# Performance work log

Hardware: AMD Instinct MI355X
Metric: run time of the kernel (lower is better)

## Reference

```python
import jax, jax.numpy as jnp
import numpy as np

T, L, B, M, E, H, A, HID, OBS = 8, 2, 512, 128, 512, 8, 16, 1024, 64
DH = E // H


def _ln(x, s, b):
    m = jnp.mean(x, axis=-1, keepdims=True)
    v = jnp.var(x, axis=-1, keepdims=True)
    return (x - m) * jax.lax.rsqrt(v + 1e-6) * s + b


def _mlp(z, w1, b1, w2, b2, w3, b3):
    z = jax.nn.relu(z @ w1 + b1)
    z = jax.nn.relu(z @ w2 + b2)
    return z @ w3 + b3


def setup_inputs() -> dict:
    key = jax.random.key(0)
    ks = jax.random.split(key, 20)
    r = lambda i, shape: jax.random.normal(ks[i], shape, jnp.float32) * 0.02
    return dict(
        memories=jax.random.normal(ks[0], (B, L, M, E), jnp.float32),
        obs=jax.random.normal(ks[1], (B, OBS), jnp.float32),
        We=r(2, (T, OBS, E)), be=jnp.zeros((T, E), jnp.float32),
        Wq=r(3, (T, L, E, E)), Wk=r(4, (T, L, E, E)), Wv=r(5, (T, L, E, E)),
        Wo=r(6, (T, L, E, E)), bo=jnp.zeros((T, L, E), jnp.float32),
        W1=r(7, (T, L, E, E)), b1=jnp.zeros((T, L, E), jnp.float32),
        W2=r(8, (T, L, E, E)), b2=jnp.zeros((T, L, E), jnp.float32),
        ln1_s=jnp.ones((T, L, E), jnp.float32), ln1_b=jnp.zeros((T, L, E), jnp.float32),
        ln2_s=jnp.ones((T, L, E), jnp.float32), ln2_b=jnp.zeros((T, L, E), jnp.float32),
        aW1=r(9, (T, E, HID)), ab1=jnp.zeros((T, HID), jnp.float32),
        aW2=r(10, (T, HID, HID)), ab2=jnp.zeros((T, HID), jnp.float32),
        aW3=r(11, (T, HID, A)), ab3=jnp.zeros((T, A), jnp.float32),
        cW1=r(12, (T, E, HID)), cb1=jnp.zeros((T, HID), jnp.float32),
        cW2=r(13, (T, HID, HID)), cb2=jnp.zeros((T, HID), jnp.float32),
        cW3=r(14, (T, HID, 1)), cb3=jnp.zeros((T, 1), jnp.float32),
        state_skills=jax.random.randint(ks[15], (B,), 0, T),
        mask=jnp.ones((B, M), dtype=bool),
    )


def reference(memories, obs, We, be, Wq, Wk, Wv, Wo, bo, W1, b1, W2, b2,
              ln1_s, ln1_b, ln2_s, ln2_b, aW1, ab1, aW2, ab2, aW3, ab3,
              cW1, cb1, cW2, cb2, cW3, cb3, state_skills, mask):
    scale = 1.0 / np.sqrt(DH)
    # current-step token is always attendable -> append True column
    fmask = jnp.concatenate([mask, jnp.ones((B, 1), dtype=bool)], axis=1)  # [B, M+1]
    xs, mems = [], []
    for t in range(T):  # dense compute over ALL tasks (as in the original)
        h = obs @ We[t] + be[t]  # [B, E]
        layer_mems = []
        for l in range(L):
            layer_mems.append(h)  # TrXL-style: memory_out = layer inputs
            kv = jnp.concatenate([memories[:, l], h[:, None, :]], axis=1)  # [B, M+1, E]
            qn = _ln(h, ln1_s[t, l], ln1_b[t, l])
            kn = _ln(kv, ln1_s[t, l], ln1_b[t, l])
            q = (qn @ Wq[t, l]).reshape(B, H, DH)
            k = (kn @ Wk[t, l]).reshape(B, M + 1, H, DH)
            v = (kn @ Wv[t, l]).reshape(B, M + 1, H, DH)
            s = jnp.einsum('bhd,bshd->bhs', q, k) * scale
            s = jnp.where(fmask[:, None, :], s, -1e9)
            p = jax.nn.softmax(s, axis=-1)
            o = jnp.einsum('bhs,bshd->bhd', p, v).reshape(B, E) @ Wo[t, l] + bo[t, l]
            h = h + o
            hn = _ln(h, ln2_s[t, l], ln2_b[t, l])
            h = h + jax.nn.relu(hn @ W1[t, l] + b1[t, l]) @ W2[t, l] + b2[t, l]
        xs.append(h)
        mems.append(jnp.stack(layer_mems, axis=1))  # [B, L, E]
    x_all = jnp.stack(xs, axis=1)       # [B, T, E]
    mem_all = jnp.stack(mems, axis=1)   # [B, T, L, E]
    onehot = jnp.eye(T, dtype=x_all.dtype)[state_skills]  # [B, T]
    x = jnp.sum(x_all * onehot[:, :, None], axis=1)                 # [B, E]
    memory_out = jnp.sum(mem_all * onehot[:, :, None, None], axis=1)  # [B, L, E]
    actor = jnp.stack([_mlp(x, aW1[t], ab1[t], aW2[t], ab2[t], aW3[t], ab3[t]) for t in range(T)], axis=1)   # [B, T, A]
    critic = jnp.stack([_mlp(x, cW1[t], cb1[t], cW2[t], cb2[t], cW3[t], cb3[t]) for t in range(T)], axis=1)  # [B, T, 1]
    logits = jnp.sum(actor * onehot[:, :, None], axis=1)                    # [B, A]
    values = jnp.sum(critic * onehot[:, :, None], axis=1).squeeze(-1)       # [B]
    return logits, values, memory_out
```

## Files before the change

kernel.cpp:

```cpp
#include <hip/hip_runtime.h>

#define TT    8
#define LLAY  2
#define BB    512
#define MM    128
#define EE    512
#define NH    8
#define HID   1024
#define NA    16
#define NOBS  64

#define OUT_LOGITS 0
#define OUT_VALUES (BB*NA)
#define OUT_MEM    (BB*NA + BB)

#define WS_H    0
#define WS_R    (WS_H + BB*EE)
#define WS_B16  (WS_R + BB*NH*EE)
#define U_F1    0
#define U_O     (U_F1 + BB*EE)
#define U_HB    (U_O  + BB*EE)
#define U_PV    (U_HB + BB*EE)
#define U_Z1A   (U_PV + BB*NH*EE)
#define U_Z2A   (U_Z1A + BB*HID)
#define U_Z1C   (U_Z2A + BB*HID)
#define U_Z2C   (U_Z1C + BB*HID)
#define U_OBSB  (U_Z2C + BB*HID)
#define U_QB    (U_OBSB + BB*NOBS)
#define U_END   (U_QB + BB*EE)
#define WS_INT  (WS_B16 + (U_END + 1)/2)

#define WI_CNT  0
#define WI_OFF  8
#define WI_MODE 17
#define WI_ROWL 32

typedef __attribute__((ext_vector_type(8))) short bf16x8;
typedef __attribute__((ext_vector_type(4))) float f32x4;

__device__ __forceinline__ float bf2f(unsigned short u) {
  return __uint_as_float(((unsigned)u) << 16);
}
__device__ __forceinline__ unsigned cvt_pk_bf16(float lo, float hi) {
  unsigned r;
  asm("v_cvt_pk_bf16_f32 %0, %1, %2" : "=v"(r) : "v"(lo), "v"(hi));
  return r;
}
__device__ __forceinline__ bf16x8 pack8(const float* f) {
  union { unsigned u[4]; bf16x8 v; } x;
  x.u[0] = cvt_pk_bf16(f[0], f[1]);
  x.u[1] = cvt_pk_bf16(f[2], f[3]);
  x.u[2] = cvt_pk_bf16(f[4], f[5]);
  x.u[3] = cvt_pk_bf16(f[6], f[7]);
  return x.v;
}

#define DPP_ADD(x, ctrl) \
  (x) += __int_as_float(__builtin_amdgcn_update_dpp(0, __float_as_int(x), (ctrl), 0xf, 0xf, true))

__device__ __forceinline__ float wave_sum(float x) {
  DPP_ADD(x, 0x121);
  DPP_ADD(x, 0x122);
  DPP_ADD(x, 0x124);
  DPP_ADD(x, 0x128);
  x += __shfl_xor(x, 16);
  x += __shfl_xor(x, 32);
  return x;
}

__device__ __forceinline__ float f4c(const float4 v, int c) {
  return c == 0 ? v.x : (c == 1 ? v.y : (c == 2 ? v.z : v.w));
}

__global__ __launch_bounds__(256) void prep_k(const int* __restrict__ skills,
                                              const void* __restrict__ mask,
                                              const float* __restrict__ obs,
                                              unsigned short* __restrict__ obsb,
                                              int* __restrict__ wsI)
{
  if (blockIdx.x > 0) {
    const int i = ((blockIdx.x - 1)*256 + threadIdx.x)*4;
    const float4 v = *(const float4*)(obs + i);
    uint2 p;
    p.x = cvt_pk_bf16(v.x, v.y);
    p.y = cvt_pk_bf16(v.z, v.w);
    *(uint2*)(obsb + i) = p;
    return;
  }
  __shared__ int cnt_s[TT];
  __shared__ int off_s[TT];
  const int tid = threadIdx.x;
  if (tid < TT) cnt_s[tid] = 0;
  __syncthreads();
  const int b0 = tid, b1i = tid + 256;
  const int t0 = skills[b0], t1 = skills[b1i];
  const int o0 = atomicAdd(&cnt_s[t0], 1);
  const int o1 = atomicAdd(&cnt_s[t1], 1);
  __syncthreads();
  if (tid == 0) {
    int off = 0;
    for (int t = 0; t < TT; ++t) {
      off_s[t] = off;
      wsI[WI_CNT + t] = cnt_s[t];
      wsI[WI_OFF + t] = off;
      off += cnt_s[t];
    }
    const unsigned char* m8 = (const unsigned char*)mask;
    const int w0 = *(const int*)mask;
    int mode = 0;
    if (m8[0] == 1 && m8[1] == 1 && m8[2] == 1 && m8[3] == 1) mode = 0;
    else if (w0 == 1) mode = 1;
    else if (w0 == 0x3f800000) mode = 2;
    wsI[WI_MODE] = mode;
  }
  __syncthreads();
  wsI[WI_ROWL + off_s[t0] + o0] = b0;
  wsI[WI_ROWL + off_s[t1] + o1] = b1i;
}

template<int KK, int KSPLIT, int RF, bool LNIN, bool RELU, bool HASBIAS, bool HASRES, bool OUTBF, bool HEADA>
__global__ __launch_bounds__((KSPLIT == 8) ? 512 : 256) void mg_k(
    const void* __restrict__ Aa, const void* __restrict__ Ab, int lda,
    const float* __restrict__ Wa, const float* __restrict__ Wb, long wStride, long wOff,
    int N,
    const float* __restrict__ biasa, const float* __restrict__ biasb, int bStride, int bOff,
    const float* __restrict__ lnS, const float* __restrict__ lnB, long lnOff,
    const float* __restrict__ res, int ldres,
    void* __restrict__ Ca, void* __restrict__ Cb_, int ldc,
    const int* __restrict__ wsI)
{
  constexpr int NW = (KSPLIT == 8) ? 8 : 4;
  constexpr int Kper = KK / KSPLIT;
  constexpr int NK = Kper / 32;
  constexpr int MR = RF * 16;
  const int t = blockIdx.z & 7, sel = blockIdx.z >> 3;
  const int cnt = wsI[WI_CNT + t];
  if (cnt == 0) return;
  const int* rowl = wsI + WI_ROWL + wsI[WI_OFF + t];
  const int tid = threadIdx.x, lane = tid & 63, w = tid >> 6;
  const int l15 = lane & 15, l4 = lane >> 4;
  const int kw    = (KSPLIT == 8) ? w : (w & 1);
  const int ntile = (KSPLIT == 8) ? 0 : (w >> 1);
  const int jbase = blockIdx.x * (KSPLIT == 8 ? 16 : 32) + ntile*16;

  const float* Wt = (sel ? Wb : Wa) + (size_t)t*wStride + wOff;
  const float* wp = Wt + (size_t)(kw*Kper + l4*8)*N + jbase + l15;

  bf16x8 afr[NK];
  #pragma unroll
  for (int kk = 0; kk < NK; ++kk) {
    float f[8];
    #pragma unroll
    for (int j = 0; j < 8; ++j) f[j] = wp[(size_t)(kk*32 + j)*N];
    afr[kk] = pack8(f);
  }

  float s1v[NK][8], b1v[NK][8];
  if constexpr (LNIN) {
    const float* sp = lnS + (size_t)t*(LLAY*EE) + lnOff + kw*Kper + l4*8;
    const float* bp = lnB + (size_t)t*(LLAY*EE) + lnOff + kw*Kper + l4*8;
    #pragma unroll
    for (int kk = 0; kk < NK; ++kk) {
      *(float4*)&s1v[kk][0] = *(const float4*)(sp + kk*32);
      *(float4*)&s1v[kk][4] = *(const float4*)(sp + kk*32 + 4);
      *(float4*)&b1v[kk][0] = *(const float4*)(bp + kk*32);
      *(float4*)&b1v[kk][4] = *(const float4*)(bp + kk*32 + 4);
    }
  }

  __shared__ __align__(16) f32x4 red_s[NW][RF][64];
  __shared__ float2 lnred_s[8][RF][16];

  for (int rb = 0; rb < cnt; rb += MR) {
    int row[RF];
    size_t abase[RF];
    #pragma unroll
    for (int rf = 0; rf < RF; ++rf) {
      row[rf] = rowl[min(rb + rf*16 + l15, cnt - 1)];
      abase[rf] = (size_t)row[rf]*lda
          + (HEADA ? (size_t)(jbase >> 6)*EE : 0) + kw*Kper + l4*8;
    }

    bf16x8 bfrv[RF][NK];
    if constexpr (LNIN) {
      float av[RF][NK][8];
      #pragma unroll
      for (int rf = 0; rf < RF; ++rf) {
        const float* apf = (const float*)(sel ? Ab : Aa) + abase[rf];
        float s = 0.f, q = 0.f;
        #pragma unroll
        for (int kk = 0; kk < NK; ++kk) {
          *(float4*)&av[rf][kk][0] = *(const float4*)(apf + kk*32);
          *(float4*)&av[rf][kk][4] = *(const float4*)(apf + kk*32 + 4);
          #pragma unroll
          for (int j = 0; j < 8; ++j) {
            s += av[rf][kk][j];
            q += av[rf][kk][j]*av[rf][kk][j];
          }
        }
        s += __shfl_xor(s, 16); s += __shfl_xor(s, 32);
        q += __shfl_xor(q, 16); q += __shfl_xor(q, 32);
        if (l4 == 0) lnred_s[w][rf][l15] = make_float2(s, q);
      }
      __syncthreads();
      #pragma unroll
      for (int rf = 0; rf < RF; ++rf) {
        float S = 0.f, Q = 0.f;
        #pragma unroll
        for (int ww = 0; ww < NW; ++ww) {
          const float2 v = lnred_s[ww][rf][l15];
          S += v.x; Q += v.y;
        }
        const float mu = S*(1.f/EE);
        const float inv = rsqrtf(Q*(1.f/EE) - mu*mu + 1e-6f);
        #pragma unroll
        for (int kk = 0; kk < NK; ++kk) {
          float f[8];
          #pragma unroll
          for (int j = 0; j < 8; ++j)
            f[j] = (av[rf][kk][j] - mu)*inv*s1v[kk][j] + b1v[kk][j];
          bfrv[rf][kk] = pack8(f);
        }
      }
    } else {
      #pragma unroll
      for (int rf = 0; rf < RF; ++rf)
        #pragma unroll
        for (int kk = 0; kk < NK; ++kk)
          bfrv[rf][kk] = *(const bf16x8*)((const unsigned short*)(sel ? Ab : Aa)
                                          + abase[rf] + kk*32);
    }

    f32x4 acc[RF];
    #pragma unroll
    for (int rf = 0; rf < RF; ++rf) acc[rf] = (f32x4){0.f, 0.f, 0.f, 0.f};
    #pragma unroll
    for (int kk = 0; kk < NK; ++kk)
      #pragma unroll
      for (int rf = 0; rf < RF; ++rf)
        acc[rf] = __builtin_amdgcn_mfma_f32_16x16x32_bf16(afr[kk], bfrv[rf][kk], acc[rf], 0, 0, 0);

    #pragma unroll
    for (int rf = 0; rf < RF; ++rf) red_s[w][rf][lane] = acc[rf];
    __syncthreads();

    if (kw == 0) {
      #pragma unroll
      for (int rf = 0; rf < RF; ++rf) {
        if (KSPLIT == 8) {
          #pragma unroll
          for (int ww = 1; ww < 8; ++ww) acc[rf] += red_s[ww][rf][lane];
        } else {
          acc[rf] += red_s[w + 1][rf][lane];
        }
        if (rb + rf*16 + l15 < cnt) {
          const int nb = jbase + l4*4;
          float vv[4];
          float4 bv, rv;
          if (HASBIAS) bv = *(const float4*)((sel ? biasb : biasa) + (size_t)t*bStride + bOff + nb);
          if (HASRES)  rv = *(const float4*)(res + (size_t)row[rf]*ldres + nb);
          #pragma unroll
          for (int c = 0; c < 4; ++c) {
            float x = acc[rf][c];
            if (HASBIAS) x += f4c(bv, c);
            if (RELU)    x = fmaxf(x, 0.f);
            if (HASRES)  x += f4c(rv, c);
            vv[c] = x;
          }
          void* C = sel ? Cb_ : Ca;
          if (OUTBF) {
            uint2 p;
            p.x = cvt_pk_bf16(vv[0], vv[1]);
            p.y = cvt_pk_bf16(vv[2], vv[3]);
            *(uint2*)((unsigned short*)C + (size_t)row[rf]*ldc + nb) = p;
          } else {
            *(float4*)((float*)C + (size_t)row[rf]*ldc + nb) = make_float4(vv[0], vv[1], vv[2], vv[3]);
          }
        }
      }
    }
    __syncthreads();
  }
}

__global__ __launch_bounds__(256) void rk_k(const unsigned short* __restrict__ qb,
                                            const float* __restrict__ Wk,
                                            float* __restrict__ R_ws,
                                            const int* __restrict__ wsI, int l)
{
  const int t = blockIdx.z & 7, h = blockIdx.z >> 3;
  const int cnt = wsI[WI_CNT + t];
  if (cnt == 0) return;
  const int* rowl = wsI + WI_ROWL + wsI[WI_OFF + t];
  const int tid = threadIdx.x, lane = tid & 63, w = tid >> 6;
  const int l15 = lane & 15, l4 = lane >> 4;
  const int kw = w & 1, ntile = w >> 1;
  const int ebase = blockIdx.x*32 + ntile*16;

  const float* wp = Wk + ((size_t)t*LLAY + l)*EE*EE
      + (size_t)(ebase + l15)*EE + h*64 + kw*32 + l4*8;
  float f[8];
  *(float4*)&f[0] = *(const float4*)wp;
  *(float4*)&f[4] = *(const float4*)(wp + 4);
  const bf16x8 afr = pack8(f);

  __shared__ __align__(16) f32x4 red_s[4][2][64];

  for (int rb = 0; rb < cnt; rb += 32) {
    int row[2];
    f32x4 acc[2];
    #pragma unroll
    for (int rf = 0; rf < 2; ++rf) {
      row[rf] = rowl[min(rb + rf*16 + l15, cnt - 1)];
      const bf16x8 bfr = *(const bf16x8*)(qb + (size_t)row[rf]*EE + h*64 + kw*32 + l4*8);
      acc[rf] = __builtin_amdgcn_mfma_f32_16x16x32_bf16(afr, bfr,
                  (f32x4){0.f,0.f,0.f,0.f}, 0, 0, 0);
    }
    #pragma unroll
    for (int rf = 0; rf < 2; ++rf) red_s[w][rf][lane] = acc[rf];
    __syncthreads();
    if (kw == 0) {
      #pragma unroll
      for (int rf = 0; rf < 2; ++rf) {
        acc[rf] += red_s[w + 1][rf][lane];
        if (rb + rf*16 + l15 < cnt) {
          const int e = ebase + l4*4;
          *(float4*)(R_ws + ((size_t)row[rf]*NH + h)*EE + e) =
              make_float4(acc[rf][0], acc[rf][1], acc[rf][2], acc[rf][3]);
        }
      }
    }
    __syncthreads();
  }
}

__global__ __launch_bounds__(256) void attn_k(const float* __restrict__ mem,
                                              const float* __restrict__ hsrc,
                                              const float* __restrict__ R_ws,
                                              const float* __restrict__ ln1s,
                                              const float* __restrict__ ln1b,
                                              const void* __restrict__ mask,
                                              const int* __restrict__ skills,
                                              const int* __restrict__ wsI,
                                              unsigned short* __restrict__ PV,
                                              float* __restrict__ memout, int l)
{
  const int b = blockIdx.x, tid = threadIdx.x;
  const int wvi = tid >> 6, lane = tid & 63;
  const int l15 = lane & 15, l4 = lane >> 4;
  const int t = skills[b];
  const int mode = wsI[WI_MODE];

  __shared__ __align__(16) float qn_l[EE];
  __shared__ __align__(16) float w_s[NH][132];
  __shared__ __align__(16) float p_s[NH][MM];
  __shared__ float mu_s[MM], inv_s[MM], S_s[MM], Q_s[MM];
  __shared__ float hsS[NH], hsA[NH], hsP[NH], hspex[NH];
  __shared__ __align__(16) unsigned short rp_bf[16][520];
  __shared__ __align__(16) float score_s[MM][20];
  __shared__ float rs_s[4], rq_s[4];

  const float* s1p = ln1s + ((size_t)t*LLAY + l)*EE;
  const float* b1p = ln1b + ((size_t)t*LLAY + l)*EE;

  {
    const float* hr = hsrc + (size_t)b*EE;
    const float x0 = hr[tid], x1 = hr[tid + 256];
    memout[((size_t)b*LLAY + l)*EE + tid] = x0;
    memout[((size_t)b*LLAY + l)*EE + tid + 256] = x1;
    float s = wave_sum(x0 + x1);
    float q = wave_sum(x0*x0 + x1*x1);
    if (lane == 0) { rs_s[wvi] = s; rq_s[wvi] = q; }
    __syncthreads();
    const float S = rs_s[0] + rs_s[1] + rs_s[2] + rs_s[3];
    const float Q = rq_s[0] + rq_s[1] + rq_s[2] + rq_s[3];
    const float mu = S*(1.f/EE);
    const float inv = rsqrtf(Q*(1.f/EE) - mu*mu + 1e-6f);
    qn_l[tid]       = (x0 - mu)*inv*s1p[tid]       + b1p[tid];
    qn_l[tid + 256] = (x1 - mu)*inv*s1p[tid + 256] + b1p[tid + 256];
  }
  __syncthreads();

  const int e8 = lane*8;
  float s1v[8], b1v[8], qnv[8];
  *(float4*)&s1v[0] = *(const float4*)(s1p + e8);
  *(float4*)&s1v[4] = *(const float4*)(s1p + e8 + 4);
  *(float4*)&b1v[0] = *(const float4*)(b1p + e8);
  *(float4*)&b1v[4] = *(const float4*)(b1p + e8 + 4);
  *(float4*)&qnv[0] = *(const float4*)&qn_l[e8];
  *(float4*)&qnv[4] = *(const float4*)&qn_l[e8 + 4];

  const float scale = 0.125f;
  float rp[NH][8];
  float SR[NH], BR[NH], SE[NH];
  #pragma unroll
  for (int h = 0; h < NH; ++h) {
    float rv[8];
    *(float4*)&rv[0] = *(const float4*)(R_ws + ((size_t)b*NH + h)*EE + e8);
    *(float4*)&rv[4] = *(const float4*)(R_ws + ((size_t)b*NH + h)*EE + e8 + 4);
    float pr = 0.f, pb = 0.f, ps = 0.f;
    #pragma unroll
    for (int j = 0; j < 8; ++j) {
      const float r = rv[j]*scale;
      const float x = r*s1v[j];
      rp[h][j] = x;
      pr += x; pb += b1v[j]*r; ps += qnv[j]*r;
    }
    SR[h] = wave_sum(pr);
    BR[h] = wave_sum(pb);
    SE[h] = wave_sum(ps);
  }

  if (wvi == 0) {
    #pragma unroll
    for (int h = 0; h < NH; ++h)
      *(bf16x8*)&rp_bf[h][e8] = pack8(rp[h]);
  } else if (wvi == 1) {
    bf16x8 ones, zer;
    #pragma unroll
    for (int j = 0; j < 8; ++j) { ones[j] = (short)0x3F80; zer[j] = 0; }
    *(bf16x8*)&rp_bf[8][e8] = ones;
    #pragma unroll
    for (int r = 9; r < 16; ++r) *(bf16x8*)&rp_bf[r][e8] = zer;
  }
  if (tid == 0) {
    #pragma unroll
    for (int h = 0; h < NH; ++h) w_s[h][MM] = SE[h];
  }
  __syncthreads();

  const float* base = mem + ((size_t)b*LLAY + l)*MM*EE;
  #pragma unroll
  for (int half = 0; half < 2; ++half) {
    const int mt = wvi + half*4;
    const int mg = mt*16 + l15;
    const float* xp = base + (size_t)mg*EE + l4*8;
    f32x4 sacc = {0.f,0.f,0.f,0.f}, gacc = {0.f,0.f,0.f,0.f};
    #pragma unroll
    for (int ks = 0; ks < 16; ++ks) {
      float f[8];
      *(float4*)&f[0] = *(const float4*)(xp + ks*32);
      *(float4*)&f[4] = *(const float4*)(xp + ks*32 + 4);
      const bf16x8 xfr = pack8(f);
      const bf16x8 afr = *(const bf16x8*)&rp_bf[l15][ks*32 + l4*8];
      sacc = __builtin_amdgcn_mfma_f32_16x16x32_bf16(afr, xfr, sacc, 0, 0, 0);
      gacc = __builtin_amdgcn_mfma_f32_16x16x32_bf16(xfr, xfr, gacc, 0, 0, 0);
    }
    if (l4 < 2) *(f32x4*)&score_s[mg][l4*4] = sacc;
    if (l4 == 2) S_s[mg] = sacc[0];
    if (l4 == (l15 >> 2)) {
      const int c = l15 & 3;
      Q_s[mg] = (c == 0) ? gacc[0] : (c == 1) ? gacc[1] : (c == 2) ? gacc[2] : gacc[3];
    }
  }
  __syncthreads();

  if (tid < MM) {
    const int m = tid;
    const float muv = S_s[m]*(1.f/EE);
    const float invv = rsqrtf(Q_s[m]*(1.f/EE) - muv*muv + 1e-6f);
    mu_s[m] = muv; inv_s[m] = invv;
    bool valid;
    if (mode == 0)      valid = ((const unsigned char*)mask)[(size_t)b*MM + m] != 0;
    else if (mode == 1) valid = ((const int*)mask)[(size_t)b*MM + m] != 0;
    else                valid = ((const float*)mask)[(size_t)b*MM + m] != 0.f;
    #pragma unroll
    for (int h = 0; h < NH; ++h) {
      const float sc = invv*score_s[m][h] - muv*invv*SR[h] + BR[h];
      const float p = valid ? __expf(sc) : 0.f;
      p_s[h][m] = p;
      w_s[h][m] = p*invv;
    }
  }
  __syncthreads();

  {
    const int h = tid >> 5, li = tid & 31;
    const float p0 = p_s[h][li], p1 = p_s[h][li+32], p2 = p_s[h][li+64], p3 = p_s[h][li+96];
    const float i0 = inv_s[li], i1 = inv_s[li+32], i2 = inv_s[li+64], i3 = inv_s[li+96];
    const float m0 = mu_s[li], m1 = mu_s[li+32], m2 = mu_s[li+64], m3 = mu_s[li+96];
    const float pe = (li == 0) ? __expf(w_s[h][MM]) : 0.f;
    float Sp = p0 + p1 + p2 + p3 + pe;
    float Ap = p0*m0*i0 + p1*m1*i1 + p2*m2*i2 + p3*m3*i3;
    float Pp = p0 + p1 + p2 + p3;
    #pragma unroll
    for (int o = 16; o; o >>= 1) {
      Sp += __shfl_xor(Sp, o);
      Ap += __shfl_xor(Ap, o);
      Pp += __shfl_xor(Pp, o);
    }
    if (li == 0) { hsS[h] = Sp; hsA[h] = Ap; hsP[h] = Pp; hspex[h] = pe; }
  }
  __syncthreads();

  const int e0 = wvi*128 + lane*2;
  const float s1x = s1p[e0], s1y = s1p[e0+1];
  const float b1x = b1p[e0], b1y = b1p[e0+1];
  const float qx = qn_l[e0], qy = qn_l[e0+1];
  float accx[NH], accy[NH];
  #pragma unroll
  for (int h = 0; h < NH; ++h) { accx[h] = 0.f; accy[h] = 0.f; }
  const float* bp2 = mem + ((size_t)b*LLAY + l)*MM*EE + e0;
  for (int m4 = 0; m4 < MM; m4 += 4) {
    float4 wv4[NH];
    #pragma unroll
    for (int h = 0; h < NH; ++h) wv4[h] = *(const float4*)&w_s[h][m4];
    #pragma unroll
    for (int c = 0; c < 4; ++c) {
      const float2 x2 = *(const float2*)(bp2 + (size_t)(m4 + c)*EE);
      #pragma unroll
      for (int h = 0; h < NH; ++h) {
        const float wv = f4c(wv4[h], c);
        accx[h] += wv*x2.x;
        accy[h] += wv*x2.y;
      }
    }
  }
  #pragma unroll
  for (int h = 0; h < NH; ++h) {
    const float is = 1.f/hsS[h];
    const float px = (s1x*(accx[h] - hsA[h]) + b1x*hsP[h] + hspex[h]*qx)*is;
    const float py = (s1y*(accy[h] - hsA[h]) + b1y*hsP[h] + hspex[h]*qy)*is;
    const unsigned pk = cvt_pk_bf16(px, py);
    *(unsigned*)(PV + ((size_t)b*NH + h)*EE + e0) = pk;
  }
}

__global__ __launch_bounds__(256) void head_k(const unsigned short* __restrict__ z2a,
                                              const unsigned short* __restrict__ z2c,
                                              const float* __restrict__ aW3,
                                              const float* __restrict__ ab3,
                                              const float* __restrict__ cW3,
                                              const float* __restrict__ cb3,
                                              const int* __restrict__ skills,
                                              float* __restrict__ out)
{
  const int b = blockIdx.x, tid = threadIdx.x;
  const int t = skills[b];
  __shared__ float za[HID], zc[HID];
  __shared__ float red[16][17];
  __shared__ float redv[4];
  for (int i = tid; i < HID; i += 256) {
    za[i] = bf2f(z2a[(size_t)b*HID + i]);
    zc[i] = bf2f(z2c[(size_t)b*HID + i]);
  }
  __syncthreads();
  {
    const int j = tid & 15, grp = tid >> 4;
    const float* w = aW3 + (size_t)t*HID*NA;
    float p = 0.f;
    for (int i = grp*64; i < grp*64 + 64; ++i) p += za[i]*w[(size_t)i*NA + j];
    red[grp][j] = p;
  }
  float pvv = 0.f;
  {
    const float* w = cW3 + (size_t)t*HID;
    for (int i = tid; i < HID; i += 256) pvv += zc[i]*w[i];
  }
  pvv = wave_sum(pvv);
  const int wvi = tid >> 6, lane = tid & 63;
  if (lane == 0) redv[wvi] = pvv;
  __syncthreads();
  if (tid < 16) {
    float v = ab3[(size_t)t*NA + tid];
    #pragma unroll
    for (int g = 0; g < 16; ++g) v += red[g][tid];
    out[OUT_LOGITS + (size_t)b*NA + tid] = v;
  }
  if (tid == 0)
    out[OUT_VALUES + b] = cb3[t] + redv[0] + redv[1] + redv[2] + redv[3];
}

extern "C" void kernel_launch(void* const* d_in, const int* in_sizes, int n_in,
                              void* d_out, int out_size, void* d_ws, size_t ws_size,
                              hipStream_t stream)
{
  (void)in_sizes; (void)n_in; (void)out_size; (void)ws_size;
  const float* memories = (const float*)d_in[0];
  const float* obs   = (const float*)d_in[1];
  const float* We    = (const float*)d_in[2];
  const float* be    = (const float*)d_in[3];
  const float* Wq    = (const float*)d_in[4];
  const float* Wk    = (const float*)d_in[5];
  const float* Wv    = (const float*)d_in[6];
  const float* Wo    = (const float*)d_in[7];
  const float* bo    = (const float*)d_in[8];
  const float* W1    = (const float*)d_in[9];
  const float* b1    = (const float*)d_in[10];
  const float* W2    = (const float*)d_in[11];
  const float* b2    = (const float*)d_in[12];
  const float* ln1s  = (const float*)d_in[13];
  const float* ln1b  = (const float*)d_in[14];
  const float* ln2s  = (const float*)d_in[15];
  const float* ln2b  = (const float*)d_in[16];
  const float* aW1   = (const float*)d_in[17];
  const float* ab1   = (const float*)d_in[18];
  const float* aW2   = (const float*)d_in[19];
  const float* ab2   = (const float*)d_in[20];
  const float* aW3   = (const float*)d_in[21];
  const float* ab3   = (const float*)d_in[22];
  const float* cW1   = (const float*)d_in[23];
  const float* cb1   = (const float*)d_in[24];
  const float* cW2   = (const float*)d_in[25];
  const float* cb2   = (const float*)d_in[26];
  const float* cW3   = (const float*)d_in[27];
  const float* cb3   = (const float*)d_in[28];
  const int*   skills= (const int*)d_in[29];
  const void*  mask  = d_in[30];

  float* ws  = (float*)d_ws;
  float* out = (float*)d_out;
  float* h   = ws + WS_H;
  float* R   = ws + WS_R;
  unsigned short* bf = (unsigned short*)(ws + WS_B16);
  unsigned short* f1   = bf + U_F1;
  unsigned short* o    = bf + U_O;
  unsigned short* hb   = bf + U_HB;
  unsigned short* PV   = bf + U_PV;
  unsigned short* z1a  = bf + U_Z1A;
  unsigned short* z2a  = bf + U_Z2A;
  unsigned short* z1c  = bf + U_Z1C;
  unsigned short* z2c  = bf + U_Z2C;
  unsigned short* obsb = bf + U_OBSB;
  unsigned short* qb   = bf + U_QB;
  int* wsI = (int*)(ws + WS_INT);

  prep_k<<<1 + BB*NOBS/1024, 256, 0, stream>>>(skills, mask, obs, obsb, wsI);

  mg_k<64,2,2,false,false,true,false,false,false><<<dim3(EE/32,1,TT), 256, 0, stream>>>(
      obsb, obsb, NOBS, We, We, (long)NOBS*EE, 0, EE,
      be, be, EE, 0, nullptr, nullptr, 0, nullptr, 0, h, h, EE, wsI);

  for (int l = 0; l < LLAY; ++l) {
    const long wOff = (long)l*EE*EE;
    mg_k<512,8,2,true,false,false,false,true,false><<<dim3(EE/16,1,TT), 512, 0, stream>>>(
        h, h, EE, Wq, Wq, (long)LLAY*EE*EE, wOff, EE,
        nullptr, nullptr, 0, 0, ln1s, ln1b, (long)l*EE, nullptr, 0, qb, qb, EE, wsI);
    rk_k<<<dim3(EE/32,1,TT*NH), 256, 0, stream>>>(qb, Wk, R, wsI, l);
    attn_k<<<BB, 256, 0, stream>>>(memories, h, R, ln1s, ln1b, mask, skills, wsI,
                                   PV, out + OUT_MEM, l);
    mg_k<512,8,2,false,false,false,false,true,true><<<dim3(EE/16,1,TT), 512, 0, stream>>>(
        PV, PV, NH*EE, Wv, Wv, (long)LLAY*EE*EE, wOff, EE,
        nullptr, nullptr, 0, 0, nullptr, nullptr, 0, nullptr, 0, o, o, EE, wsI);
    mg_k<512,8,2,false,false,true,true,false,false><<<dim3(EE/16,1,TT), 512, 0, stream>>>(
        o, o, EE, Wo, Wo, (long)LLAY*EE*EE, wOff, EE,
        bo, bo, LLAY*EE, l*EE, nullptr, nullptr, 0, h, EE, h, h, EE, wsI);
    mg_k<512,8,2,true,true,true,false,true,false><<<dim3(EE/16,1,TT), 512, 0, stream>>>(
        h, h, EE, W1, W1, (long)LLAY*EE*EE, wOff, EE,
        b1, b1, LLAY*EE, l*EE, ln2s, ln2b, (long)l*EE, nullptr, 0, f1, f1, EE, wsI);
    if (l == LLAY - 1) {
      mg_k<512,8,2,false,false,true,true,true,false><<<dim3(EE/16,1,TT), 512, 0, stream>>>(
          f1, f1, EE, W2, W2, (long)LLAY*EE*EE, wOff, EE,
          b2, b2, LLAY*EE, l*EE, nullptr, nullptr, 0, h, EE, hb, hb, EE, wsI);
    } else {
      mg_k<512,8,2,false,false,true,true,false,false><<<dim3(EE/16,1,TT), 512, 0, stream>>>(
          f1, f1, EE, W2, W2, (long)LLAY*EE*EE, wOff, EE,
          b2, b2, LLAY*EE, l*EE, nullptr, nullptr, 0, h, EE, h, h, EE, wsI);
    }
  }

  mg_k<512,8,4,false,true,true,false,true,false><<<dim3(HID/16,1,2*TT), 512, 0, stream>>>(
      hb, hb, EE, aW1, cW1, (long)EE*HID, 0, HID,
      ab1, cb1, HID, 0, nullptr, nullptr, 0, nullptr, 0, z1a, z1c, HID, wsI);
  mg_k<1024,8,4,false,true,true,false,true,false><<<dim3(HID/16,1,2*TT), 512, 0, stream>>>(
      z1a, z1c, HID, aW2, cW2, (long)HID*HID, 0, HID,
      ab2, cb2, HID, 0, nullptr, nullptr, 0, nullptr, 0, z2a, z2c, HID, wsI);

  head_k<<<BB, 256, 0, stream>>>(z2a, z2c, aW3, ab3, cW3, cb3, skills, out);
}
```

Baseline: 316.1 us.

## Double-buffer memory tiles into LDS with async loads in attention scoring

```diff
diff --git a/kernel.cpp b/kernel.cpp
--- a/kernel.cpp
+++ b/kernel.cpp
@@ -53,6 +53,13 @@
   x.u[2] = cvt_pk_bf16(f[4], f[5]);
   x.u[3] = cvt_pk_bf16(f[6], f[7]);
   return x.v;
+}
+
+__device__ __forceinline__ void async_cp16(const void* gsrc, void* ldsdst) {
+  __builtin_amdgcn_global_load_lds(
+      (const __attribute__((address_space(1))) unsigned int*)gsrc,
+      (__attribute__((address_space(3))) unsigned int*)ldsdst,
+      16, 0, 0);
 }
 
 #define DPP_ADD(x, ctrl) \
@@ -351,6 +358,7 @@
   const int t = skills[b];
   const int mode = wsI[WI_MODE];
 
+  __shared__ __align__(16) float xs_s[2][16*512];
   __shared__ __align__(16) float qn_l[EE];
   __shared__ __align__(16) float w_s[NH][132];
   __shared__ __align__(16) float p_s[NH][MM];
@@ -359,6 +367,25 @@
   __shared__ __align__(16) unsigned short rp_bf[16][520];
   __shared__ __align__(16) float score_s[MM][20];
   __shared__ float rs_s[4], rq_s[4];
+  __shared__ __align__(16) f32x4 red_sa[4][64];
+  __shared__ __align__(16) f32x4 red_ga[4][64];
+
+  const float* base = mem + ((size_t)b*LLAY + l)*MM*EE;
+
+  #define STAGE_TILE(TILE, BUF)                                            \
+    {                                                                      \
+      const char* gt_ = (const char*)(base + (size_t)(TILE)*16*EE);        \
+      char* lt_ = (char*)&xs_s[(BUF)][0];                                  \
+      _Pragma("unroll")                                                    \
+      for (int i_ = 0; i_ < 8; ++i_) {                                     \
+        const int X_ = wvi*1024 + i_*4096 + lane*16;                       \
+        const int m_ = X_ >> 11;                                           \
+        const int off_ = (X_ & 2047) ^ ((m_ & 7) << 4);                    \
+        async_cp16(gt_ + (m_ << 11) + off_, lt_ + wvi*1024 + i_*4096);     \
+      }                                                                    \
+    }
+
+  STAGE_TILE(0, 0)
 
   const float* s1p = ln1s + ((size_t)t*LLAY + l)*EE;
   const float* b1p = ln1b + ((size_t)t*LLAY + l)*EE;
@@ -429,31 +456,42 @@
   }
   __syncthreads();
 
-  const float* base = mem + ((size_t)b*LLAY + l)*MM*EE;
-  #pragma unroll
-  for (int half = 0; half < 2; ++half) {
-    const int mt = wvi + half*4;
-    const int mg = mt*16 + l15;
-    const float* xp = base + (size_t)mg*EE + l4*8;
+  for (int tile = 0; tile < 8; ++tile) {
+    const int buf = tile & 1;
+    asm volatile("s_waitcnt vmcnt(0)" ::: "memory");
+    __syncthreads();
+    if (tile + 1 < 8) STAGE_TILE(tile + 1, buf ^ 1)
+
     f32x4 sacc = {0.f,0.f,0.f,0.f}, gacc = {0.f,0.f,0.f,0.f};
     #pragma unroll
-    for (int ks = 0; ks < 16; ++ks) {
+    for (int kq = 0; kq < 4; ++kq) {
+      const int ks = wvi*4 + kq;
+      const int boff = (l15*2048 + ((ks*128 + l4*32) ^ ((l15 & 7) << 4))) >> 2;
       float f[8];
-      *(float4*)&f[0] = *(const float4*)(xp + ks*32);
-      *(float4*)&f[4] = *(const float4*)(xp + ks*32 + 4);
+      *(float4*)&f[0] = *(const float4*)&xs_s[buf][boff];
+      *(float4*)&f[4] = *(const float4*)&xs_s[buf][boff + 4];
       const bf16x8 xfr = pack8(f);
       const bf16x8 afr = *(const bf16x8*)&rp_bf[l15][ks*32 + l4*8];
       sacc = __builtin_amdgcn_mfma_f32_16x16x32_bf16(afr, xfr, sacc, 0, 0, 0);
       gacc = __builtin_amdgcn_mfma_f32_16x16x32_bf16(xfr, xfr, gacc, 0, 0, 0);
     }
-    if (l4 < 2) *(f32x4*)&score_s[mg][l4*4] = sacc;
-    if (l4 == 2) S_s[mg] = sacc[0];
-    if (l4 == (l15 >> 2)) {
-      const int c = l15 & 3;
-      Q_s[mg] = (c == 0) ? gacc[0] : (c == 1) ? gacc[1] : (c == 2) ? gacc[2] : gacc[3];
-    }
-  }
-  __syncthreads();
+    red_sa[wvi][lane] = sacc;
+    red_ga[wvi][lane] = gacc;
+    __syncthreads();
+    if (wvi == 0) {
+      f32x4 s = red_sa[0][lane], g = red_ga[0][lane];
+      #pragma unroll
+      for (int ww = 1; ww < 4; ++ww) { s += red_sa[ww][lane]; g += red_ga[ww][lane]; }
+      const int mg = tile*16 + l15;
+      if (l4 < 2) *(f32x4*)&score_s[mg][l4*4] = s;
+      if (l4 == 2) S_s[mg] = s[0];
+      if (l4 == (l15 >> 2)) {
+        const int c = l15 & 3;
+        Q_s[mg] = (c == 0) ? g[0] : (c == 1) ? g[1] : (c == 2) ? g[2] : g[3];
+      }
+    }
+    __syncthreads();
+  }
 
   if (tid < MM) {
     const int m = tid;
@@ -524,6 +562,7 @@
     const unsigned pk = cvt_pk_bf16(px, py);
     *(unsigned*)(PV + ((size_t)b*NH + h)*EE + e0) = pk;
   }
+  #undef STAGE_TILE
 }
 
 __global__ __launch_bounds__(256) void head_k(const unsigned short* __restrict__ z2a,
```

Measured after the change: 354.8 us. +12.3%, slower.

## Compute attention P·V with MFMA and fuse softmax stats into score epilogue

Applied to the files above, without the earlier changes.

```diff
diff --git a/kernel.cpp b/kernel.cpp
--- a/kernel.cpp
+++ b/kernel.cpp
@@ -352,12 +352,10 @@
   const int mode = wsI[WI_MODE];
 
   __shared__ __align__(16) float qn_l[EE];
-  __shared__ __align__(16) float w_s[NH][132];
-  __shared__ __align__(16) float p_s[NH][MM];
-  __shared__ float mu_s[MM], inv_s[MM], S_s[MM], Q_s[MM];
-  __shared__ float hsS[NH], hsA[NH], hsP[NH], hspex[NH];
   __shared__ __align__(16) unsigned short rp_bf[16][520];
-  __shared__ __align__(16) float score_s[MM][20];
+  __shared__ __align__(16) unsigned short wT_s[4][2][8][16];
+  __shared__ float2 SpAp_s[4][8];
+  __shared__ __align__(16) float mrg_s[2][8][128];
   __shared__ float rs_s[4], rq_s[4];
 
   const float* s1p = ln1s + ((size_t)t*LLAY + l)*EE;
@@ -423,13 +421,10 @@
     #pragma unroll
     for (int r = 9; r < 16; ++r) *(bf16x8*)&rp_bf[r][e8] = zer;
   }
-  if (tid == 0) {
-    #pragma unroll
-    for (int h = 0; h < NH; ++h) w_s[h][MM] = SE[h];
-  }
   __syncthreads();
 
   const float* base = mem + ((size_t)b*LLAY + l)*MM*EE;
+  float spAcc[4] = {0.f,0.f,0.f,0.f}, apAcc[4] = {0.f,0.f,0.f,0.f};
   #pragma unroll
   for (int half = 0; half < 2; ++half) {
     const int mt = wvi + half*4;
@@ -446,83 +441,119 @@
       sacc = __builtin_amdgcn_mfma_f32_16x16x32_bf16(afr, xfr, sacc, 0, 0, 0);
       gacc = __builtin_amdgcn_mfma_f32_16x16x32_bf16(xfr, xfr, gacc, 0, 0, 0);
     }
-    if (l4 < 2) *(f32x4*)&score_s[mg][l4*4] = sacc;
-    if (l4 == 2) S_s[mg] = sacc[0];
-    if (l4 == (l15 >> 2)) {
-      const int c = l15 & 3;
-      Q_s[mg] = (c == 0) ? gacc[0] : (c == 1) ? gacc[1] : (c == 2) ? gacc[2] : gacc[3];
-    }
+    const float Sm = __shfl(sacc[0], 32 + l15);
+    const int srcL = 16*(l15 >> 2) + l15;
+    const float q0 = __shfl(gacc[0], srcL);
+    const float q1 = __shfl(gacc[1], srcL);
+    const float q2 = __shfl(gacc[2], srcL);
+    const float q3 = __shfl(gacc[3], srcL);
+    const int qs = l15 & 3;
+    const float Qm = qs == 0 ? q0 : (qs == 1 ? q1 : (qs == 2 ? q2 : q3));
+    const float muv = Sm*(1.f/EE);
+    const float invv = rsqrtf(Qm*(1.f/EE) - muv*muv + 1e-6f);
+    bool valid;
+    if (mode == 0)      valid = ((const unsigned char*)mask)[(size_t)b*MM + mg] != 0;
+    else if (mode == 1) valid = ((const int*)mask)[(size_t)b*MM + mg] != 0;
+    else                valid = ((const float*)mask)[(size_t)b*MM + mg] != 0.f;
+    if (l4 < 2) {
+      #pragma unroll
+      for (int c = 0; c < 4; ++c) {
+        const float SRh = l4 ? SR[c + 4] : SR[c];
+        const float BRh = l4 ? BR[c + 4] : BR[c];
+        const float sc = invv*sacc[c] - muv*invv*SRh + BRh;
+        const float p = valid ? __expf(sc) : 0.f;
+        spAcc[c] += p;
+        apAcc[c] += p*muv*invv;
+        wT_s[wvi][half][l4*4 + c][l15] =
+            (unsigned short)(cvt_pk_bf16(p*invv, p*invv) & 0xffffu);
+      }
+    }
+  }
+
+  #pragma unroll
+  for (int o = 1; o <= 8; o <<= 1) {
+    #pragma unroll
+    for (int c = 0; c < 4; ++c) {
+      spAcc[c] += __shfl_xor(spAcc[c], o);
+      apAcc[c] += __shfl_xor(apAcc[c], o);
+    }
+  }
+  if (l4 < 2 && l15 == 0) {
+    #pragma unroll
+    for (int c = 0; c < 4; ++c)
+      SpAp_s[wvi][l4*4 + c] = make_float2(spAcc[c], apAcc[c]);
   }
   __syncthreads();
 
-  if (tid < MM) {
-    const int m = tid;
-    const float muv = S_s[m]*(1.f/EE);
-    const float invv = rsqrtf(Q_s[m]*(1.f/EE) - muv*muv + 1e-6f);
-    mu_s[m] = muv; inv_s[m] = invv;
-    bool valid;
-    if (mode == 0)      valid = ((const unsigned char*)mask)[(size_t)b*MM + m] != 0;
-    else if (mode == 1) valid = ((const int*)mask)[(size_t)b*MM + m] != 0;
-    else                valid = ((const float*)mask)[(size_t)b*MM + m] != 0.f;
-    #pragma unroll
-    for (int h = 0; h < NH; ++h) {
-      const float sc = invv*score_s[m][h] - muv*invv*SR[h] + BR[h];
-      const float p = valid ? __expf(sc) : 0.f;
-      p_s[h][m] = p;
-      w_s[h][m] = p*invv;
-    }
-  }
-  __syncthreads();
-
-  {
-    const int h = tid >> 5, li = tid & 31;
-    const float p0 = p_s[h][li], p1 = p_s[h][li+32], p2 = p_s[h][li+64], p3 = p_s[h][li+96];
-    const float i0 = inv_s[li], i1 = inv_s[li+32], i2 = inv_s[li+64], i3 = inv_s[li+96];
-    const float m0 = mu_s[li], m1 = mu_s[li+32], m2 = mu_s[li+64], m3 = mu_s[li+96];
-    const float pe = (li == 0) ? __expf(w_s[h][MM]) : 0.f;
-    float Sp = p0 + p1 + p2 + p3 + pe;
-    float Ap = p0*m0*i0 + p1*m1*i1 + p2*m2*i2 + p3*m3*i3;
-    float Pp = p0 + p1 + p2 + p3;
-    #pragma unroll
-    for (int o = 16; o; o >>= 1) {
-      Sp += __shfl_xor(Sp, o);
-      Ap += __shfl_xor(Ap, o);
-      Pp += __shfl_xor(Pp, o);
-    }
-    if (li == 0) { hsS[h] = Sp; hsA[h] = Ap; hsP[h] = Pp; hspex[h] = pe; }
-  }
-  __syncthreads();
-
-  const int e0 = wvi*128 + lane*2;
-  const float s1x = s1p[e0], s1y = s1p[e0+1];
-  const float b1x = b1p[e0], b1y = b1p[e0+1];
-  const float qx = qn_l[e0], qy = qn_l[e0+1];
-  float accx[NH], accy[NH];
-  #pragma unroll
-  for (int h = 0; h < NH; ++h) { accx[h] = 0.f; accy[h] = 0.f; }
-  const float* bp2 = mem + ((size_t)b*LLAY + l)*MM*EE + e0;
-  for (int m4 = 0; m4 < MM; m4 += 4) {
-    float4 wv4[NH];
-    #pragma unroll
-    for (int h = 0; h < NH; ++h) wv4[h] = *(const float4*)&w_s[h][m4];
+  float Sp_h[4], Ap_h[4], pe_h[4], is_h[4];
+  if (wvi == 0 && l4 < 2) {
     #pragma unroll
     for (int c = 0; c < 4; ++c) {
-      const float2 x2 = *(const float2*)(bp2 + (size_t)(m4 + c)*EE);
-      #pragma unroll
-      for (int h = 0; h < NH; ++h) {
-        const float wv = f4c(wv4[h], c);
-        accx[h] += wv*x2.x;
-        accy[h] += wv*x2.y;
+      const int h = l4*4 + c;
+      float sp = 0.f, ap = 0.f;
+      #pragma unroll
+      for (int w2 = 0; w2 < 4; ++w2) { sp += SpAp_s[w2][h].x; ap += SpAp_s[w2][h].y; }
+      const float SEh = l4 ? SE[c + 4] : SE[c];
+      const float pe = __expf(SEh);
+      Sp_h[c] = sp; Ap_h[c] = ap; pe_h[c] = pe; is_h[c] = 1.f/(sp + pe);
+    }
+  }
+
+  const bf16x8 afr_pv = *(const bf16x8*)&wT_s[wvi][l4 >> 1][l15 & 7][(l4 & 1)*8];
+  const int tile_sel = (l4 >> 1) ? (wvi + 4) : wvi;
+  const float* xb = base + (size_t)(tile_sel*16 + (l4 & 1)*8)*EE + l15;
+
+  for (int q = 0; q < 4; ++q) {
+    f32x4 Uq[8];
+    #pragma unroll
+    for (int ns = 0; ns < 8; ++ns) {
+      const int e0 = (q*8 + ns)*16;
+      float f[8];
+      #pragma unroll
+      for (int j = 0; j < 8; ++j) f[j] = xb[(size_t)j*EE + e0];
+      Uq[ns] = __builtin_amdgcn_mfma_f32_16x16x32_bf16(afr_pv, pack8(f),
+                 (f32x4){0.f,0.f,0.f,0.f}, 0, 0, 0);
+    }
+    if ((wvi == 1 || wvi == 3) && l4 < 2) {
+      const int mb = wvi >> 1;
+      #pragma unroll
+      for (int ns = 0; ns < 8; ++ns)
+        #pragma unroll
+        for (int c = 0; c < 4; ++c)
+          mrg_s[mb][l4*4 + c][ns*16 + l15] = Uq[ns][c];
+    }
+    __syncthreads();
+    if ((wvi == 0 || wvi == 2) && l4 < 2) {
+      const int mb = wvi >> 1;
+      #pragma unroll
+      for (int ns = 0; ns < 8; ++ns)
+        #pragma unroll
+        for (int c = 0; c < 4; ++c)
+          Uq[ns][c] += mrg_s[mb][l4*4 + c][ns*16 + l15];
+    }
+    if (wvi == 2 && l4 < 2) {
+      #pragma unroll
+      for (int ns = 0; ns < 8; ++ns)
+        #pragma unroll
+        for (int c = 0; c < 4; ++c)
+          mrg_s[1][l4*4 + c][ns*16 + l15] = Uq[ns][c];
+    }
+    __syncthreads();
+    if (wvi == 0 && l4 < 2) {
+      #pragma unroll
+      for (int ns = 0; ns < 8; ++ns) {
+        const int e = (q*8 + ns)*16 + l15;
+        const float s1e = s1p[e], b1e = b1p[e], qne = qn_l[e];
+        #pragma unroll
+        for (int c = 0; c < 4; ++c) {
+          const float U = Uq[ns][c] + mrg_s[1][l4*4 + c][ns*16 + l15];
+          const float px = (s1e*(U - Ap_h[c]) + b1e*Sp_h[c] + pe_h[c]*qne)*is_h[c];
+          PV[((size_t)b*NH + (l4*4 + c))*EE + e] =
+              (unsigned short)(cvt_pk_bf16(px, px) & 0xffffu);
+        }
       }
     }
-  }
-  #pragma unroll
-  for (int h = 0; h < NH; ++h) {
-    const float is = 1.f/hsS[h];
-    const float px = (s1x*(accx[h] - hsA[h]) + b1x*hsP[h] + hspex[h]*qx)*is;
-    const float py = (s1y*(accy[h] - hsA[h]) + b1y*hsP[h] + hspex[h]*qy)*is;
-    const unsigned pk = cvt_pk_bf16(px, py);
-    *(unsigned*)(PV + ((size_t)b*NH + h)*EE + e0) = pk;
+    __syncthreads();
   }
 }
 
```

Result: slower. 378.1 us (+19.6%).
